# Performance work log

Measured on AMD Instinct MI355X. Metric: run time of the kernel, lower is better.

Reference implementation:

```python
import jax, jax.numpy as jnp
import numpy as np

N = 50000      # nodes
E = 600000     # edges
G = 256        # graphs in batch
H = 128        # hidden channels
EPS = 1e-5     # batchnorm eps


def gcn_conv(x, W, b, src, dst, n):
    """PyG GCNConv: h = x W; symmetric-normalized aggregation with self-loops."""
    h = x @ W  # [n, H]
    ones = jnp.ones(src.shape[0], dtype=x.dtype)
    deg = jax.ops.segment_sum(ones, dst, num_segments=n) + 1.0  # in-degree + self-loop
    dis = jax.lax.rsqrt(deg)  # deg^{-1/2}
    msg = (dis[src] * dis[dst])[:, None] * h[src]  # [E, H] gathered messages
    agg = jax.ops.segment_sum(msg, dst, num_segments=n)
    return agg + (dis * dis)[:, None] * h + b  # self-loop contribution + bias


def batch_norm(x, gamma, beta):
    m = x.mean(axis=0)
    v = x.var(axis=0)  # biased variance, as torch BN uses for normalization
    return gamma * (x - m) * jax.lax.rsqrt(v + EPS) + beta


def setup_inputs() -> dict:
    key = jax.random.key(0)
    ks = jax.random.split(key, 12)
    x = jax.random.normal(ks[0], (N, H), dtype=jnp.float32)
    edge_index = jax.random.randint(ks[1], (2, E), 0, N, dtype=jnp.int32)
    batch = jnp.sort(jax.random.randint(ks[2], (N,), 0, G, dtype=jnp.int32))
    s = 1.0 / np.sqrt(H)
    W1 = jax.random.uniform(ks[3], (H, H), jnp.float32, -s, s)
    b1 = jnp.zeros((H,), jnp.float32)
    g1 = jnp.ones((H,), jnp.float32)
    be1 = jnp.zeros((H,), jnp.float32)
    W2 = jax.random.uniform(ks[4], (H, H), jnp.float32, -s, s)
    b2 = jnp.zeros((H,), jnp.float32)
    g2 = jnp.ones((H,), jnp.float32)
    be2 = jnp.zeros((H,), jnp.float32)
    W3 = jax.random.uniform(ks[5], (H, H), jnp.float32, -s, s)
    b3 = jnp.zeros((H,), jnp.float32)
    Wl = jax.random.uniform(ks[6], (H, 1), jnp.float32, -s, s)
    bl = jnp.zeros((1,), jnp.float32)
    return {"x": x, "edge_index": edge_index, "batch": batch,
            "W1": W1, "b1": b1, "g1": g1, "be1": be1,
            "W2": W2, "b2": b2, "g2": g2, "be2": be2,
            "W3": W3, "b3": b3, "Wl": Wl, "bl": bl}


def reference(x, edge_index, batch, W1, b1, g1, be1, W2, b2, g2, be2, W3, b3, Wl, bl):
    src, dst = edge_index[0], edge_index[1]
    h = gcn_conv(x, W1, b1, src, dst, N)
    h = jax.nn.relu(batch_norm(h, g1, be1))  # dropout is identity in eval mode
    h = gcn_conv(h, W2, b2, src, dst, N)
    h = jax.nn.relu(batch_norm(h, g2, be2))
    h = jax.nn.relu(gcn_conv(h, W3, b3, src, dst, N))
    sums = jax.ops.segment_sum(h, batch, num_segments=G)           # [G, H]
    cnt = jax.ops.segment_sum(jnp.ones((N,), h.dtype), batch, num_segments=G)
    pooled = sums / jnp.maximum(cnt, 1.0)[:, None]                  # global mean pool
    return pooled @ Wl + bl                                         # [G, 1]
```

## Files before the change

### kernel.cpp

```cpp
#include <hip/hip_runtime.h>
#include <cstdint>

#define NN 50000
#define NE 600000
#define NGR 256
#define HD 128
#define HD2 64
#define BN_EPS 1e-5f

typedef __attribute__((ext_vector_type(8))) short bf16x8;
typedef __attribute__((ext_vector_type(4))) float f32x4;

static __device__ __forceinline__ unsigned f2bf(float f) {
  unsigned u = __float_as_uint(f);
  return (u + 0x7FFFu + ((u >> 16) & 1u)) >> 16;
}
static __device__ __forceinline__ float bf_lo(unsigned v) {
  return __uint_as_float(v << 16);
}
static __device__ __forceinline__ float bf_hi(unsigned v) {
  return __uint_as_float(v & 0xFFFF0000u);
}

__global__ void k_zero(float4* __restrict__ p, int n4) {
  int i = blockIdx.x * blockDim.x + threadIdx.x;
  if (i < n4) p[i] = make_float4(0.f, 0.f, 0.f, 0.f);
}

__global__ void k_count(const int* __restrict__ dst, int* __restrict__ cnt) {
  int i = blockIdx.x * blockDim.x + threadIdx.x;
  if (i < NE) atomicAdd(&cnt[dst[i]], 1);
}

__global__ void k_bcount(const int* __restrict__ batch, float* __restrict__ gcnt) {
  int i = blockIdx.x * blockDim.x + threadIdx.x;
  if (i < NN) atomicAdd(&gcnt[batch[i]], 1.0f);
}

__global__ __launch_bounds__(1024) void k_scan1(const int* __restrict__ cnt,
                                                int* __restrict__ rowptr,
                                                int* __restrict__ aux,
                                                float* __restrict__ dis) {
  __shared__ int sd[1024];
  int tid = threadIdx.x;
  int i = blockIdx.x * 1024 + tid;
  int v = (i < NN) ? cnt[i] : 0;
  if (i < NN) dis[i] = 1.0f / sqrtf((float)v + 1.0f);
  sd[tid] = v;
  __syncthreads();
  for (int off = 1; off < 1024; off <<= 1) {
    int t = (tid >= off) ? sd[tid - off] : 0;
    __syncthreads();
    sd[tid] += t;
    __syncthreads();
  }
  if (i < NN) rowptr[i + 1] = sd[tid];
  if (tid == 1023) aux[blockIdx.x] = sd[1023];
}

__global__ void k_scan2(const int* __restrict__ aux, int* __restrict__ auxsc, int nchunks) {
  if (threadIdx.x == 0 && blockIdx.x == 0) {
    int run = 0;
    for (int c = 0; c < nchunks; ++c) { auxsc[c] = run; run += aux[c]; }
  }
}

__global__ void k_scan3(int* __restrict__ rowptr, const int* __restrict__ auxsc) {
  int i = blockIdx.x * blockDim.x + threadIdx.x;
  if (i < NN) rowptr[i + 1] += auxsc[i >> 10];
  if (i == 0) rowptr[0] = 0;
}

__global__ void k_fill(const int* __restrict__ src, const int* __restrict__ dst,
                       const int* __restrict__ rowptr, int* __restrict__ fillp,
                       int* __restrict__ colidx) {
  int i = blockIdx.x * blockDim.x + threadIdx.x;
  if (i < NE) {
    int d = dst[i];
    int p = rowptr[d] + atomicAdd(&fillp[d], 1);
    colidx[p] = src[i];
  }
}

__global__ void k_wt(const float* __restrict__ W, unsigned short* __restrict__ WT) {
  int idx = blockIdx.x * 256 + threadIdx.x;
  int k = idx >> 7, n = idx & 127;
  WT[n * 128 + k] = (unsigned short)f2bf(W[idx]);
}

template<bool BN>
__global__ __launch_bounds__(256) void k_gemm(
    const void* __restrict__ Xv, const unsigned short* __restrict__ WT,
    const float* __restrict__ scale, const float* __restrict__ shift,
    const float* __restrict__ dis, unsigned* __restrict__ HS) {
  __shared__ unsigned short lw[128 * 128];
  __shared__ unsigned short lx[128 * 128];
  int tid = threadIdx.x;
  int row0 = blockIdx.x * 128;
#pragma unroll
  for (int i = 0; i < 8; ++i) {
    int c2 = tid + 256 * i;
    int n = c2 >> 4, c = c2 & 15;
    uint4 v = *(const uint4*)&WT[n * 128 + c * 8];
    *(uint4*)&lw[n * 128 + ((c ^ (n & 15)) << 3)] = v;
  }
#pragma unroll
  for (int i = 0; i < 8; ++i) {
    int c2 = tid + 256 * i;
    int m = c2 >> 4, c = c2 & 15;
    int row = row0 + m;
    unsigned short h[8];
    if (row < NN) {
      if constexpr (!BN) {
        const float* X = (const float*)Xv;
        const float* xp = &X[(size_t)row * HD + c * 8];
        float4 a0 = *(const float4*)xp;
        float4 a1 = *(const float4*)(xp + 4);
        h[0] = (unsigned short)f2bf(a0.x); h[1] = (unsigned short)f2bf(a0.y);
        h[2] = (unsigned short)f2bf(a0.z); h[3] = (unsigned short)f2bf(a0.w);
        h[4] = (unsigned short)f2bf(a1.x); h[5] = (unsigned short)f2bf(a1.y);
        h[6] = (unsigned short)f2bf(a1.z); h[7] = (unsigned short)f2bf(a1.w);
      } else {
        const unsigned* X = (const unsigned*)Xv;
        uint4 pw = *(const uint4*)&X[(size_t)row * HD2 + c * 4];
        float4 sc0 = *(const float4*)&scale[c * 8];
        float4 sc1 = *(const float4*)&scale[c * 8 + 4];
        float4 sh0 = *(const float4*)&shift[c * 8];
        float4 sh1 = *(const float4*)&shift[c * 8 + 4];
        h[0] = (unsigned short)f2bf(fmaxf(fmaf(sc0.x, bf_lo(pw.x), sh0.x), 0.f));
        h[1] = (unsigned short)f2bf(fmaxf(fmaf(sc0.y, bf_hi(pw.x), sh0.y), 0.f));
        h[2] = (unsigned short)f2bf(fmaxf(fmaf(sc0.z, bf_lo(pw.y), sh0.z), 0.f));
        h[3] = (unsigned short)f2bf(fmaxf(fmaf(sc0.w, bf_hi(pw.y), sh0.w), 0.f));
        h[4] = (unsigned short)f2bf(fmaxf(fmaf(sc1.x, bf_lo(pw.z), sh1.x), 0.f));
        h[5] = (unsigned short)f2bf(fmaxf(fmaf(sc1.y, bf_hi(pw.z), sh1.y), 0.f));
        h[6] = (unsigned short)f2bf(fmaxf(fmaf(sc1.z, bf_lo(pw.w), sh1.z), 0.f));
        h[7] = (unsigned short)f2bf(fmaxf(fmaf(sc1.w, bf_hi(pw.w), sh1.w), 0.f));
      }
    } else {
#pragma unroll
      for (int j = 0; j < 8; ++j) h[j] = 0;
    }
    *(uint4*)&lx[m * 128 + ((c ^ (m & 15)) << 3)] = *(uint4*)h;
  }
  __syncthreads();

  int l = tid & 63, w = tid >> 6;
  int cl = l & 15, g = l >> 4;
  f32x4 acc[2][8];
#pragma unroll
  for (int mb = 0; mb < 2; ++mb)
#pragma unroll
    for (int nb = 0; nb < 8; ++nb)
#pragma unroll
      for (int z = 0; z < 4; ++z) acc[mb][nb][z] = 0.f;

#pragma unroll
  for (int ks = 0; ks < 4; ++ks) {
    int chunk = ((ks * 4 + g) ^ cl) << 3;
    bf16x8 b0 = *(bf16x8*)&lx[(w * 32 + cl) * 128 + chunk];
    bf16x8 b1 = *(bf16x8*)&lx[(w * 32 + 16 + cl) * 128 + chunk];
#pragma unroll
    for (int nb = 0; nb < 8; ++nb) {
      bf16x8 a = *(bf16x8*)&lw[(nb * 16 + cl) * 128 + chunk];
      acc[0][nb] = __builtin_amdgcn_mfma_f32_16x16x32_bf16(a, b0, acc[0][nb], 0, 0, 0);
      acc[1][nb] = __builtin_amdgcn_mfma_f32_16x16x32_bf16(a, b1, acc[1][nb], 0, 0, 0);
    }
  }
#pragma unroll
  for (int mb = 0; mb < 2; ++mb) {
    int m = row0 + w * 32 + mb * 16 + cl;
    if (m < NN) {
      float dv = dis[m];
#pragma unroll
      for (int nb = 0; nb < 8; ++nb) {
        unsigned w0 = (f2bf(acc[mb][nb][1] * dv) << 16) | f2bf(acc[mb][nb][0] * dv);
        unsigned w1 = (f2bf(acc[mb][nb][3] * dv) << 16) | f2bf(acc[mb][nb][2] * dv);
        *(uint2*)&HS[(size_t)m * HD2 + nb * 8 + g * 2] = make_uint2(w0, w1);
      }
    }
  }
}

template<int MODE>
__global__ __launch_bounds__(256) void k_agg(
    const unsigned* __restrict__ HS, const float* __restrict__ dis,
    const int* __restrict__ rowptr, const int* __restrict__ colidx,
    const float* __restrict__ bias,
    unsigned* __restrict__ AGG, float* __restrict__ stats,
    const int* __restrict__ batch, const float* __restrict__ Wl,
    float* __restrict__ gsum) {
  __shared__ float red[4][128];
  int tid = threadIdx.x;
  int lane = tid & 63;
  int wv = tid >> 6;
  int c0 = lane * 2;
  float b0 = bias[c0], b1 = bias[c0 + 1];
  float wl0 = 0.f, wl1 = 0.f;
  if (MODE == 1) { wl0 = Wl[c0]; wl1 = Wl[c0 + 1]; }
  float ssum0 = 0.f, ssum1 = 0.f, ssq0 = 0.f, ssq1 = 0.f;
  int stride = gridDim.x * 4;
  for (int i = blockIdx.x * 4 + wv; i < NN; i += stride) {
    unsigned sv = HS[(size_t)i * HD2 + lane];
    float ax = bf_lo(sv), ay = bf_hi(sv);
    float bx = 0.f, by = 0.f;
    float cx = 0.f, cy = 0.f;
    float dx = 0.f, dy = 0.f;
    int e0 = rowptr[i], e1 = rowptr[i + 1];
    int e = e0;
    for (; e < e1 && (e & 3); ++e) {
      unsigned h0 = HS[(size_t)colidx[e] * HD2 + lane];
      ax += bf_lo(h0); ay += bf_hi(h0);
    }
    for (; e + 7 < e1; e += 8) {
      int4 ca = *(const int4*)&colidx[e];
      int4 cb = *(const int4*)&colidx[e + 4];
      unsigned h0 = HS[(size_t)ca.x * HD2 + lane];
      unsigned h1 = HS[(size_t)ca.y * HD2 + lane];
      unsigned h2 = HS[(size_t)ca.z * HD2 + lane];
      unsigned h3 = HS[(size_t)ca.w * HD2 + lane];
      unsigned h4 = HS[(size_t)cb.x * HD2 + lane];
      unsigned h5 = HS[(size_t)cb.y * HD2 + lane];
      unsigned h6 = HS[(size_t)cb.z * HD2 + lane];
      unsigned h7 = HS[(size_t)cb.w * HD2 + lane];
      ax += bf_lo(h0); ay += bf_hi(h0);
      bx += bf_lo(h1); by += bf_hi(h1);
      cx += bf_lo(h2); cy += bf_hi(h2);
      dx += bf_lo(h3); dy += bf_hi(h3);
      ax += bf_lo(h4); ay += bf_hi(h4);
      bx += bf_lo(h5); by += bf_hi(h5);
      cx += bf_lo(h6); cy += bf_hi(h6);
      dx += bf_lo(h7); dy += bf_hi(h7);
    }
    for (; e + 3 < e1; e += 4) {
      int4 ca = *(const int4*)&colidx[e];
      unsigned h0 = HS[(size_t)ca.x * HD2 + lane];
      unsigned h1 = HS[(size_t)ca.y * HD2 + lane];
      unsigned h2 = HS[(size_t)ca.z * HD2 + lane];
      unsigned h3 = HS[(size_t)ca.w * HD2 + lane];
      ax += bf_lo(h0); ay += bf_hi(h0);
      bx += bf_lo(h1); by += bf_hi(h1);
      cx += bf_lo(h2); cy += bf_hi(h2);
      dx += bf_lo(h3); dy += bf_hi(h3);
    }
    for (; e < e1; ++e) {
      unsigned h0 = HS[(size_t)colidx[e] * HD2 + lane];
      ax += bf_lo(h0); ay += bf_hi(h0);
    }
    float di = dis[i];
    float vx = fmaf(di, (ax + bx) + (cx + dx), b0);
    float vy = fmaf(di, (ay + by) + (cy + dy), b1);
    if (MODE == 0) {
      AGG[(size_t)i * HD2 + lane] = (f2bf(vy) << 16) | f2bf(vx);
      ssum0 += vx; ssum1 += vy;
      ssq0 = fmaf(vx, vx, ssq0);
      ssq1 = fmaf(vy, vy, ssq1);
    } else {
      vx = fmaxf(vx, 0.f);
      vy = fmaxf(vy, 0.f);
      float p = vx * wl0 + vy * wl1;
#pragma unroll
      for (int m = 32; m >= 1; m >>= 1) p += __shfl_xor(p, m);
      if (lane == 0) atomicAdd(&gsum[batch[i]], p);
    }
  }
  if (MODE == 0) {
    red[wv][c0] = ssum0; red[wv][c0 + 1] = ssum1;
    __syncthreads();
    if (wv == 0) {
      float t0 = red[0][c0] + red[1][c0] + red[2][c0] + red[3][c0];
      float t1 = red[0][c0 + 1] + red[1][c0 + 1] + red[2][c0 + 1] + red[3][c0 + 1];
      atomicAdd(&stats[c0], t0);
      atomicAdd(&stats[c0 + 1], t1);
    }
    __syncthreads();
    red[wv][c0] = ssq0; red[wv][c0 + 1] = ssq1;
    __syncthreads();
    if (wv == 0) {
      float q0 = red[0][c0] + red[1][c0] + red[2][c0] + red[3][c0];
      float q1 = red[0][c0 + 1] + red[1][c0 + 1] + red[2][c0 + 1] + red[3][c0 + 1];
      atomicAdd(&stats[HD + c0], q0);
      atomicAdd(&stats[HD + c0 + 1], q1);
    }
  }
}

__global__ void k_bnfin(const float* __restrict__ stats, const float* __restrict__ gamma,
                        const float* __restrict__ beta, float* __restrict__ scale,
                        float* __restrict__ shift) {
  int c = threadIdx.x;
  float inv_n = 1.0f / (float)NN;
  float mean = stats[c] * inv_n;
  float var = stats[HD + c] * inv_n - mean * mean;
  float s = gamma[c] / sqrtf(var + BN_EPS);
  scale[c] = s;
  shift[c] = fmaf(-mean, s, beta[c]);
}

__global__ void k_final(const float* __restrict__ gsum, const float* __restrict__ gcnt,
                        const float* __restrict__ bl, float* __restrict__ out) {
  int g = threadIdx.x;
  out[g] = gsum[g] / fmaxf(gcnt[g], 1.0f) + bl[0];
}

extern "C" void kernel_launch(void* const* d_in, const int* in_sizes, int n_in,
                              void* d_out, int out_size, void* d_ws, size_t ws_size,
                              hipStream_t stream) {
  (void)in_sizes; (void)n_in; (void)out_size; (void)ws_size;
  const float* x   = (const float*)d_in[0];
  const int* ei    = (const int*)d_in[1];
  const int* batch = (const int*)d_in[2];
  const float* W1  = (const float*)d_in[3];
  const float* b1  = (const float*)d_in[4];
  const float* g1  = (const float*)d_in[5];
  const float* be1 = (const float*)d_in[6];
  const float* W2  = (const float*)d_in[7];
  const float* b2  = (const float*)d_in[8];
  const float* g2  = (const float*)d_in[9];
  const float* be2 = (const float*)d_in[10];
  const float* W3  = (const float*)d_in[11];
  const float* b3  = (const float*)d_in[12];
  const float* Wl  = (const float*)d_in[13];
  const float* bl  = (const float*)d_in[14];
  float* out = (float*)d_out;

  const int* srcv = ei;
  const int* dstv = ei + NE;

  unsigned* hs   = (unsigned*)d_ws;
  unsigned* aggb = hs + (size_t)NN * HD2;
  float* dis     = (float*)(aggb + (size_t)NN * HD2);
  int*   rowptr  = (int*)(dis + NN);
  int*   colidx  = rowptr + (NN + 4);
  unsigned short* wtb = (unsigned short*)(colidx + NE);
  float* scale1  = (float*)(wtb + 128 * 128);
  float* shift1  = scale1 + HD;
  float* scale2  = shift1 + HD;
  float* shift2  = scale2 + HD;
  float* zbase   = shift2 + HD;
  int*   degc    = (int*)zbase;
  int*   fillp   = degc + NN;
  int*   aux     = fillp + NN;
  int*   auxsc   = aux + 64;
  float* stats1  = (float*)(auxsc + 64);
  float* stats2  = stats1 + 2 * HD;
  float* gsum    = stats2 + 2 * HD;
  float* gcnt    = gsum + NGR;
  float* zend    = gcnt + NGR;
  int n4 = (int)(((char*)zend - (char*)zbase) / 16);

  k_zero<<<(n4 + 255) / 256, 256, 0, stream>>>((float4*)zbase, n4);

  k_count<<<(NE + 255) / 256, 256, 0, stream>>>(dstv, degc);
  k_bcount<<<(NN + 255) / 256, 256, 0, stream>>>(batch, gcnt);
  int nchunk = (NN + 1023) / 1024;
  k_scan1<<<nchunk, 1024, 0, stream>>>(degc, rowptr, aux, dis);
  k_scan2<<<1, 1, 0, stream>>>(aux, auxsc, nchunk);
  k_scan3<<<(NN + 255) / 256, 256, 0, stream>>>(rowptr, auxsc);
  k_fill<<<(NE + 255) / 256, 256, 0, stream>>>(srcv, dstv, rowptr, fillp, colidx);

  int gblk = (NN + 127) / 128;
  k_wt<<<64, 256, 0, stream>>>(W1, wtb);
  k_gemm<false><<<gblk, 256, 0, stream>>>(x, wtb, nullptr, nullptr, dis, hs);
  k_agg<0><<<2048, 256, 0, stream>>>(hs, dis, rowptr, colidx, b1, aggb, stats1,
                                     nullptr, nullptr, nullptr);
  k_bnfin<<<1, HD, 0, stream>>>(stats1, g1, be1, scale1, shift1);
  k_wt<<<64, 256, 0, stream>>>(W2, wtb);
  k_gemm<true><<<gblk, 256, 0, stream>>>(aggb, wtb, scale1, shift1, dis, hs);
  k_agg<0><<<2048, 256, 0, stream>>>(hs, dis, rowptr, colidx, b2, aggb, stats2,
                                     nullptr, nullptr, nullptr);
  k_bnfin<<<1, HD, 0, stream>>>(stats2, g2, be2, scale2, shift2);
  k_wt<<<64, 256, 0, stream>>>(W3, wtb);
  k_gemm<true><<<gblk, 256, 0, stream>>>(aggb, wtb, scale2, shift2, dis, hs);
  k_agg<1><<<2048, 256, 0, stream>>>(hs, dis, rowptr, colidx, b3, nullptr, nullptr,
                                     batch, Wl, gsum);
  k_final<<<1, NGR, 0, stream>>>(gsum, gcnt, bl, out);
}
```

Before: 759.4 us.

## Add paired-node aggregation kernel and halve GEMM row tile

```diff
diff --git a/kernel.cpp b/kernel.cpp
--- a/kernel.cpp
+++ b/kernel.cpp
@@ -94,9 +94,9 @@
     const float* __restrict__ scale, const float* __restrict__ shift,
     const float* __restrict__ dis, unsigned* __restrict__ HS) {
   __shared__ unsigned short lw[128 * 128];
-  __shared__ unsigned short lx[128 * 128];
+  __shared__ unsigned short lx[64 * 128];
   int tid = threadIdx.x;
-  int row0 = blockIdx.x * 128;
+  int row0 = blockIdx.x * 64;
 #pragma unroll
   for (int i = 0; i < 8; ++i) {
     int c2 = tid + 256 * i;
@@ -105,7 +105,7 @@
     *(uint4*)&lw[n * 128 + ((c ^ (n & 15)) << 3)] = v;
   }
 #pragma unroll
-  for (int i = 0; i < 8; ++i) {
+  for (int i = 0; i < 4; ++i) {
     int c2 = tid + 256 * i;
     int m = c2 >> 4, c = c2 & 15;
     int row = row0 + m;
@@ -146,38 +146,101 @@
 
   int l = tid & 63, w = tid >> 6;
   int cl = l & 15, g = l >> 4;
-  f32x4 acc[2][8];
-#pragma unroll
-  for (int mb = 0; mb < 2; ++mb)
-#pragma unroll
-    for (int nb = 0; nb < 8; ++nb)
-#pragma unroll
-      for (int z = 0; z < 4; ++z) acc[mb][nb][z] = 0.f;
+  f32x4 acc[8];
+#pragma unroll
+  for (int nb = 0; nb < 8; ++nb)
+#pragma unroll
+    for (int z = 0; z < 4; ++z) acc[nb][z] = 0.f;
 
 #pragma unroll
   for (int ks = 0; ks < 4; ++ks) {
     int chunk = ((ks * 4 + g) ^ cl) << 3;
-    bf16x8 b0 = *(bf16x8*)&lx[(w * 32 + cl) * 128 + chunk];
-    bf16x8 b1 = *(bf16x8*)&lx[(w * 32 + 16 + cl) * 128 + chunk];
+    bf16x8 b = *(bf16x8*)&lx[(w * 16 + cl) * 128 + chunk];
 #pragma unroll
     for (int nb = 0; nb < 8; ++nb) {
       bf16x8 a = *(bf16x8*)&lw[(nb * 16 + cl) * 128 + chunk];
-      acc[0][nb] = __builtin_amdgcn_mfma_f32_16x16x32_bf16(a, b0, acc[0][nb], 0, 0, 0);
-      acc[1][nb] = __builtin_amdgcn_mfma_f32_16x16x32_bf16(a, b1, acc[1][nb], 0, 0, 0);
-    }
-  }
-#pragma unroll
-  for (int mb = 0; mb < 2; ++mb) {
-    int m = row0 + w * 32 + mb * 16 + cl;
-    if (m < NN) {
-      float dv = dis[m];
-#pragma unroll
-      for (int nb = 0; nb < 8; ++nb) {
-        unsigned w0 = (f2bf(acc[mb][nb][1] * dv) << 16) | f2bf(acc[mb][nb][0] * dv);
-        unsigned w1 = (f2bf(acc[mb][nb][3] * dv) << 16) | f2bf(acc[mb][nb][2] * dv);
-        *(uint2*)&HS[(size_t)m * HD2 + nb * 8 + g * 2] = make_uint2(w0, w1);
-      }
-    }
+      acc[nb] = __builtin_amdgcn_mfma_f32_16x16x32_bf16(a, b, acc[nb], 0, 0, 0);
+    }
+  }
+  int m = row0 + w * 16 + cl;
+  if (m < NN) {
+    float dv = dis[m];
+#pragma unroll
+    for (int nb = 0; nb < 8; ++nb) {
+      unsigned w0 = (f2bf(acc[nb][1] * dv) << 16) | f2bf(acc[nb][0] * dv);
+      unsigned w1 = (f2bf(acc[nb][3] * dv) << 16) | f2bf(acc[nb][2] * dv);
+      *(uint2*)&HS[(size_t)m * HD2 + nb * 8 + g * 2] = make_uint2(w0, w1);
+    }
+  }
+}
+
+__global__ __launch_bounds__(256) void k_aggp(
+    const unsigned* __restrict__ HS, const float* __restrict__ dis,
+    const int* __restrict__ rowptr, const int* __restrict__ colidx,
+    const float* __restrict__ bias, unsigned* __restrict__ AGG,
+    float* __restrict__ stats) {
+  __shared__ float red[8][128];
+  int tid = threadIdx.x;
+  int lane = tid & 63;
+  int wv = tid >> 6;
+  int il = lane & 31;
+  int half = lane >> 5;
+  int c0 = il * 4;
+  float4 bi = *(const float4*)&bias[c0];
+  float s0 = 0.f, s1 = 0.f, s2 = 0.f, s3 = 0.f;
+  float q0 = 0.f, q1 = 0.f, q2 = 0.f, q3 = 0.f;
+  int stride = gridDim.x * 4;
+  for (int p = blockIdx.x * 4 + wv; p < NN / 2; p += stride) {
+    int n = p * 2 + half;
+    int e0 = rowptr[n], e1 = rowptr[n + 1];
+    int deg = e1 - e0;
+    int m = max(deg, __shfl_xor(deg, 32));
+    uint2 sv = *(const uint2*)&HS[(size_t)n * HD2 + il * 2];
+    float a0 = bf_lo(sv.x), a1 = bf_hi(sv.x);
+    float a2 = bf_lo(sv.y), a3 = bf_hi(sv.y);
+    float b0 = 0.f, b1 = 0.f, b2 = 0.f, b3 = 0.f;
+    int ecl = max(e1 - 1, 0);
+    for (int k = 0; k < m; k += 2) {
+      int eA = e0 + k, eB = e0 + k + 1;
+      int iA = colidx[min(eA, ecl)];
+      int iB = colidx[min(eB, ecl)];
+      uint2 hA = *(const uint2*)&HS[(size_t)iA * HD2 + il * 2];
+      uint2 hB = *(const uint2*)&HS[(size_t)iB * HD2 + il * 2];
+      if (eA >= e1) { hA.x = 0u; hA.y = 0u; }
+      if (eB >= e1) { hB.x = 0u; hB.y = 0u; }
+      a0 += bf_lo(hA.x); a1 += bf_hi(hA.x);
+      a2 += bf_lo(hA.y); a3 += bf_hi(hA.y);
+      b0 += bf_lo(hB.x); b1 += bf_hi(hB.x);
+      b2 += bf_lo(hB.y); b3 += bf_hi(hB.y);
+    }
+    float di = dis[n];
+    float v0 = fmaf(di, a0 + b0, bi.x);
+    float v1 = fmaf(di, a1 + b1, bi.y);
+    float v2 = fmaf(di, a2 + b2, bi.z);
+    float v3 = fmaf(di, a3 + b3, bi.w);
+    *(uint2*)&AGG[(size_t)n * HD2 + il * 2] =
+        make_uint2((f2bf(v1) << 16) | f2bf(v0), (f2bf(v3) << 16) | f2bf(v2));
+    s0 += v0; s1 += v1; s2 += v2; s3 += v3;
+    q0 = fmaf(v0, v0, q0); q1 = fmaf(v1, v1, q1);
+    q2 = fmaf(v2, v2, q2); q3 = fmaf(v3, v3, q3);
+  }
+  int r = wv * 2 + half;
+  *(float4*)&red[r][c0] = make_float4(s0, s1, s2, s3);
+  __syncthreads();
+  if (tid < 128) {
+    float s = 0.f;
+#pragma unroll
+    for (int r2 = 0; r2 < 8; ++r2) s += red[r2][tid];
+    atomicAdd(&stats[tid], s);
+  }
+  __syncthreads();
+  *(float4*)&red[r][c0] = make_float4(q0, q1, q2, q3);
+  __syncthreads();
+  if (tid < 128) {
+    float s = 0.f;
+#pragma unroll
+    for (int r2 = 0; r2 < 8; ++r2) s += red[r2][tid];
+    atomicAdd(&stats[HD + tid], s);
   }
 }
 
@@ -276,10 +339,10 @@
     red[wv][c0] = ssq0; red[wv][c0 + 1] = ssq1;
     __syncthreads();
     if (wv == 0) {
-      float q0 = red[0][c0] + red[1][c0] + red[2][c0] + red[3][c0];
-      float q1 = red[0][c0 + 1] + red[1][c0 + 1] + red[2][c0 + 1] + red[3][c0 + 1];
-      atomicAdd(&stats[HD + c0], q0);
-      atomicAdd(&stats[HD + c0 + 1], q1);
+      float t0 = red[0][c0] + red[1][c0] + red[2][c0] + red[3][c0];
+      float t1 = red[0][c0 + 1] + red[1][c0 + 1] + red[2][c0 + 1] + red[3][c0 + 1];
+      atomicAdd(&stats[HD + c0], t0);
+      atomicAdd(&stats[HD + c0 + 1], t1);
     }
   }
 }
@@ -358,11 +421,10 @@
   k_scan3<<<(NN + 255) / 256, 256, 0, stream>>>(rowptr, auxsc);
   k_fill<<<(NE + 255) / 256, 256, 0, stream>>>(srcv, dstv, rowptr, fillp, colidx);
 
-  int gblk = (NN + 127) / 128;
+  int gblk = (NN + 63) / 64;
   k_wt<<<64, 256, 0, stream>>>(W1, wtb);
   k_gemm<false><<<gblk, 256, 0, stream>>>(x, wtb, nullptr, nullptr, dis, hs);
-  k_agg<0><<<2048, 256, 0, stream>>>(hs, dis, rowptr, colidx, b1, aggb, stats1,
-                                     nullptr, nullptr, nullptr);
+  k_aggp<<<2048, 256, 0, stream>>>(hs, dis, rowptr, colidx, b1, aggb, stats1);
   k_bnfin<<<1, HD, 0, stream>>>(stats1, g1, be1, scale1, shift1);
   k_wt<<<64, 256, 0, stream>>>(W2, wtb);
   k_gemm<true><<<gblk, 256, 0, stream>>>(aggb, wtb, scale1, shift1, dis, hs);
```

Result: faster. 711.0 us (-6.4%).
